# Kernel optimization log

Hardware: AMD Instinct MI355X
Metric: run time of the kernel (lower is better)

Reference implementation:

```python
import jax, jax.numpy as jnp
import numpy as np

SIGMA = 0.1
B = 1.0
EPS = 1e-5


def setup_inputs() -> dict:
    key = jax.random.key(0)
    k1, k2 = jax.random.split(key)
    featureT = jax.random.normal(k1, (2, 256, 64, 64), dtype=jnp.float32)
    featureI = jax.random.normal(k2, (2, 256, 64, 64), dtype=jnp.float32)
    return {"featureT": featureT, "featureI": featureI}


def reference(featureT, featureI):
    # NCHW -> NHWC
    fI = jnp.transpose(featureI, (0, 2, 3, 1))
    fT = jnp.transpose(featureT, (0, 2, 3, 1))
    # center both by target mean over N, H, W (shape [1,1,1,C])
    meanT = fT.mean(axis=(0, 1, 2), keepdims=True)
    fI = fI - meanT
    fT = fT - meanT
    # channelwise L2 normalize
    fI = fI / jnp.linalg.norm(fI, axis=3, keepdims=True)
    fT = fT / jnp.linalg.norm(fT, axis=3, keepdims=True)
    N, H, W, C = fT.shape
    P = H * W
    # conv2d with 1x1 target patches == cosine similarity vs every target patch
    Tp = fT.reshape(N, P, C)                       # [N, P, C]
    dist = jnp.einsum('nhwc,npc->nhwp', fI, Tp)    # [N, H, W, P]
    raw_dist = (1.0 - dist) / 2.0
    # relative distance: divide by min over target-patch axis
    rel = raw_dist / (jnp.min(raw_dist, axis=3, keepdims=True) + EPS)
    # exp weighting, normalized over target-patch axis
    Wt = jnp.exp((B - rel) / SIGMA)
    CX = Wt / Wt.sum(axis=3, keepdims=True)        # [N, H, W, P]
    # max over spatial (query) dims, mean over target patches, -log, mean
    CX = CX.max(axis=2).max(axis=1)                # [N, P]
    CX = -jnp.log(CX.mean(axis=1))                 # [N]
    return jnp.mean(CX)
```

## Files before the change

kernel.cpp:

```cpp
#include <hip/hip_runtime.h>
#include <hip/hip_bf16.h>
#include <math.h>

#define NB 2
#define C 256
#define P 4096
#define EPS_F 1e-5f

typedef __attribute__((ext_vector_type(8))) short short8;
typedef __attribute__((ext_vector_type(4))) float f32x4;

__device__ __forceinline__ float bf2f(unsigned short u) {
    union { unsigned int i; float f; } x;
    x.i = ((unsigned int)u) << 16;
    return x.f;
}

__global__ void k_mean(const float* __restrict__ fT, float* __restrict__ mean) {
    int c = blockIdx.x;
    int t = threadIdx.x;
    const float* p0 = fT + (size_t)c * P;
    const float* p1 = fT + (size_t)(C + c) * P;
    float s = 0.f;
    for (int i = t; i < P; i += 256) s += p0[i] + p1[i];
    __shared__ float red[256];
    red[t] = s; __syncthreads();
    for (int o = 128; o > 0; o >>= 1) { if (t < o) red[t] += red[t + o]; __syncthreads(); }
    if (t == 0) mean[c] = red[0] * (1.f / 8192.f);
}

__global__ __launch_bounds__(256) void k_normpack(const float* __restrict__ fI,
                                                  const float* __restrict__ fT,
                                                  const float* __restrict__ mean,
                                                  __hip_bfloat16* __restrict__ TI,
                                                  __hip_bfloat16* __restrict__ TT) {
    __shared__ float mn[C];
    __shared__ float tile[C][33];
    __shared__ float part[8][32];
    __shared__ float srn[32];
    int t = threadIdx.x;
    const float* f = blockIdx.z ? fT : fI;
    __hip_bfloat16* out = blockIdx.z ? TT : TI;
    mn[t] = mean[t];
    __syncthreads();
    int n = blockIdx.y, p0 = blockIdx.x * 32;
    int pl = t & 31, cg = t >> 5;
    const float* base = f + (size_t)n * C * P + p0 + pl;
    float acc = 0.f;
    #pragma unroll 4
    for (int cc = 0; cc < 32; cc++) {
        int c = cg * 32 + cc;
        float v = base[(size_t)c * P] - mn[c];
        tile[c][pl] = v;
        acc += v * v;
    }
    part[cg][pl] = acc;
    __syncthreads();
    if (t < 32) {
        float s = 0.f;
        #pragma unroll
        for (int g = 0; g < 8; g++) s += part[g][t];
        srn[t] = rsqrtf(s);
    }
    __syncthreads();
    #pragma unroll
    for (int it = 0; it < 4; it++) {
        int flat = it * 2048 + t * 8;
        int p = flat >> 8;
        int c = flat & 255;
        float rn = srn[p];
        union { __hip_bfloat16 h[8]; short8 s; } u;
        #pragma unroll
        for (int k = 0; k < 8; k++)
            u.h[k] = __float2bfloat16(tile[c + k][p] * rn);
        *(short8*)(out + ((size_t)(n * P + p0 + p)) * C + c) = u.s;
    }
}

__device__ __forceinline__ void stage_tile(const __hip_bfloat16* __restrict__ gbase,
                                           __hip_bfloat16* lbuf, int kk, int wid, int lane) {
    #pragma unroll
    for (int j = 0; j < 2; j++) {
        int row = wid * 32 + j * 16 + (lane >> 2);
        int cb = (lane & 3) * 16;
        int scb = cb ^ (((row >> 1) & 3) << 4);
        const char* gp = (const char*)gbase + (size_t)row * (C * 2) + kk * 64 + scb;
        char* lp = (char*)lbuf + (wid * 32 + j * 16) * 64;
        __builtin_amdgcn_global_load_lds(
            (const __attribute__((address_space(1))) void*)gp,
            (__attribute__((address_space(3))) void*)lp, 16, 0, 0);
    }
}

__device__ __forceinline__ short8 ldfrag(const __hip_bfloat16* lbuf, int rloc, int kb) {
    int addr = rloc * 64 + (kb ^ (((rloc >> 1) & 3) << 4));
    return *(const short8*)((const char*)lbuf + addr);
}

__global__ __launch_bounds__(256, 3) void k_gemm(const __hip_bfloat16* __restrict__ TI,
                                                 const __hip_bfloat16* __restrict__ TT,
                                                 __hip_bfloat16* __restrict__ D,
                                                 float* __restrict__ Mpart) {
    __shared__ char smem[49152];
    int lane = threadIdx.x & 63, wid = threadIdx.x >> 6;
    int wr = wid >> 1, wc = wid & 1;
    int n = blockIdx.z;
    const __hip_bfloat16* A = TI + ((size_t)n * P + blockIdx.y * 128) * C;
    const __hip_bfloat16* B = TT + ((size_t)n * P + blockIdx.x * 128) * C;

    f32x4 acc[4][4];
    #pragma unroll
    for (int m = 0; m < 4; m++)
        #pragma unroll
        for (int nt = 0; nt < 4; nt++)
            acc[m][nt] = (f32x4){0.f, 0.f, 0.f, 0.f};

    int rA = lane & 15;
    int kb = (lane >> 4) * 16;

    stage_tile(A, (__hip_bfloat16*)(smem), 0, wid, lane);
    stage_tile(B, (__hip_bfloat16*)(smem + 24576), 0, wid, lane);
    stage_tile(A, (__hip_bfloat16*)(smem + 8192), 1, wid, lane);
    stage_tile(B, (__hip_bfloat16*)(smem + 24576 + 8192), 1, wid, lane);
    asm volatile("s_waitcnt vmcnt(4)" ::: "memory");
    __builtin_amdgcn_s_barrier();
    __builtin_amdgcn_sched_barrier(0);

    #pragma unroll
    for (int t = 0; t < 8; t++) {
        int cur = t % 3;
        if (t < 6) {
            int nxt = (t + 2) % 3;
            stage_tile(A, (__hip_bfloat16*)(smem + nxt * 8192), t + 2, wid, lane);
            stage_tile(B, (__hip_bfloat16*)(smem + 24576 + nxt * 8192), t + 2, wid, lane);
        }
        __hip_bfloat16* lAc = (__hip_bfloat16*)(smem + cur * 8192);
        __hip_bfloat16* lBc = (__hip_bfloat16*)(smem + 24576 + cur * 8192);
        short8 a[4], b[4];
        #pragma unroll
        for (int m = 0; m < 4; m++)
            a[m] = ldfrag(lAc, wr * 64 + m * 16 + rA, kb);
        #pragma unroll
        for (int nt = 0; nt < 4; nt++)
            b[nt] = ldfrag(lBc, wc * 64 + nt * 16 + rA, kb);
        #pragma unroll
        for (int m = 0; m < 4; m++)
            #pragma unroll
            for (int nt = 0; nt < 4; nt++)
                acc[m][nt] = __builtin_amdgcn_mfma_f32_16x16x32_bf16(a[m], b[nt], acc[m][nt], 0, 0, 0);
        if (t < 6)       asm volatile("s_waitcnt vmcnt(4)" ::: "memory");
        else if (t == 6) asm volatile("s_waitcnt vmcnt(0)" ::: "memory");
        __builtin_amdgcn_s_barrier();
        __builtin_amdgcn_sched_barrier(0);
    }

    int rj = (lane >> 4) * 4, cl = lane & 15;
    {
        char* tb = smem;
        #pragma unroll
        for (int m = 0; m < 4; m++)
            #pragma unroll
            for (int nt = 0; nt < 4; nt++)
                #pragma unroll
                for (int j = 0; j < 4; j++) {
                    int row = wr * 64 + m * 16 + rj + j;
                    int colb = (wc * 64 + nt * 16 + cl) * 2;
                    *(__hip_bfloat16*)(tb + row * 256 + (colb ^ (((row >> 2) & 3) << 5))) =
                        __float2bfloat16(acc[m][nt][j]);
                }
        __syncthreads();
        int qb0 = blockIdx.y * 128, pb0 = blockIdx.x * 128;
        char* Dn = (char*)(D + (size_t)n * P * P);
        #pragma unroll
        for (int rb = 0; rb < 8; rb++) {
            int row = wid * 32 + rb * 4 + (lane >> 4);
            int sb = cl * 16;
            short8 v = *(const short8*)(tb + row * 256 + (sb ^ (((row >> 2) & 3) << 5)));
            *(short8*)(Dn + ((size_t)(qb0 + row) * P + pb0) * 2 + sb) = v;
        }
    }

    int qb = blockIdx.y * 128 + wr * 64;
    int pt = blockIdx.x * 2 + wc;
    #pragma unroll
    for (int m = 0; m < 4; m++) {
        f32x4 mx = acc[m][0];
        #pragma unroll
        for (int nt = 1; nt < 4; nt++)
            #pragma unroll
            for (int j = 0; j < 4; j++)
                mx[j] = fmaxf(mx[j], acc[m][nt][j]);
        #pragma unroll
        for (int j = 0; j < 4; j++)
            #pragma unroll
            for (int o = 1; o < 16; o <<= 1)
                mx[j] = fmaxf(mx[j], __shfl_xor(mx[j], o));
        if ((lane & 15) == 0) {
            int qbase = qb + m * 16 + (lane >> 4) * 4;
            #pragma unroll
            for (int j = 0; j < 4; j++)
                Mpart[((size_t)(n * P + qbase + j)) * 64 + pt] = mx[j];
        }
    }
}

__global__ __launch_bounds__(512) void k_zcol(const __hip_bfloat16* __restrict__ D,
                                              const float* __restrict__ Mpart,
                                              float* __restrict__ Cpart) {
    __shared__ float st2[8], sc[8];
    int t = threadIdx.x, lane = t & 63, wv = t >> 6;
    int n = blockIdx.y, g = blockIdx.x;

    float cm[8];
    #pragma unroll
    for (int j = 0; j < 8; j++) cm[j] = -1e30f;

    #pragma unroll
    for (int s = 0; s < 2; s++) {
        int q = g * 16 + s * 8 + wv;
        size_t row = (size_t)n * P + q;
        float m = Mpart[row * 64 + lane];
        #pragma unroll
        for (int o = 32; o > 0; o >>= 1) m = fmaxf(m, __shfl_xor(m, o));
        float t2 = 5.f / ((1.f - m) * 0.5f + EPS_F);

        const short8* src = (const short8*)(D + row * P);
        float z = 0.f;
        #pragma unroll
        for (int k = 0; k < 8; k++) {
            short8 v = src[k * 64 + lane];
            #pragma unroll
            for (int j = 0; j < 8; j++)
                z += __expf(t2 * (bf2f((unsigned short)v[j]) - m));
        }
        #pragma unroll
        for (int o = 32; o > 0; o >>= 1) z += __shfl_xor(z, o);
        if (lane == 0) { st2[wv] = t2; sc[wv] = -t2 * m - logf(z); }
        __syncthreads();

        const __hip_bfloat16* Db = D + ((size_t)n * P + g * 16 + s * 8) * P;
        #pragma unroll
        for (int r = 0; r < 8; r++) {
            short8 v = *(const short8*)(Db + (size_t)r * P + t * 8);
            float tt = st2[r], cc = sc[r];
            #pragma unroll
            for (int j = 0; j < 8; j++)
                cm[j] = fmaxf(cm[j], fmaf(tt, bf2f((unsigned short)v[j]), cc));
        }
        __syncthreads();
    }

    float* cp = Cpart + ((size_t)(n * 256 + g)) * P + t * 8;
    f32x4 v0 = {cm[0], cm[1], cm[2], cm[3]};
    f32x4 v1 = {cm[4], cm[5], cm[6], cm[7]};
    *(f32x4*)cp = v0;
    *(f32x4*)(cp + 4) = v1;
}

__global__ void k_colred1(const float* __restrict__ Cpart, float* __restrict__ Cred2) {
    int np = blockIdx.x * 256 + threadIdx.x;
    int n = np >> 12, p = np & 4095;
    const float* base = Cpart + (size_t)(n * 256) * P + p;
    float c = -1e30f;
    int g0 = blockIdx.y * 32;
    #pragma unroll 8
    for (int g = 0; g < 32; g++)
        c = fmaxf(c, base[(size_t)(g0 + g) * P]);
    Cred2[blockIdx.y * 8192 + np] = c;
}

__global__ void k_colred2(const float* __restrict__ Cred2, float* __restrict__ colmax) {
    int np = blockIdx.x * 256 + threadIdx.x;
    float c = -1e30f;
    #pragma unroll
    for (int y = 0; y < 8; y++)
        c = fmaxf(c, Cred2[y * 8192 + np]);
    colmax[np] = __expf(c);
}

__global__ void k_final(const float* __restrict__ colmax, float* __restrict__ out) {
    __shared__ float red[256];
    int t = threadIdx.x;
    float cx[NB];
    for (int n = 0; n < NB; n++) {
        float s = 0.f;
        for (int i = t; i < P; i += 256) s += colmax[n * P + i];
        red[t] = s; __syncthreads();
        for (int o = 128; o > 0; o >>= 1) { if (t < o) red[t] += red[t + o]; __syncthreads(); }
        cx[n] = -logf(red[0] * (1.f / (float)P));
        __syncthreads();
    }
    if (t == 0) out[0] = 0.5f * (cx[0] + cx[1]);
}

extern "C" void kernel_launch(void* const* d_in, const int* in_sizes, int n_in,
                              void* d_out, int out_size, void* d_ws, size_t ws_size,
                              hipStream_t stream) {
    const float* fT = (const float*)d_in[0];
    const float* fI = (const float*)d_in[1];
    float* out = (float*)d_out;

    char* ws = (char*)d_ws;
    size_t off = 0;
    __hip_bfloat16* TI = (__hip_bfloat16*)(ws + off); off += 4194304;
    __hip_bfloat16* TT = (__hip_bfloat16*)(ws + off); off += 4194304;
    __hip_bfloat16* D  = (__hip_bfloat16*)(ws + off); off += (size_t)NB * P * P * 2;
    float* Mpart  = (float*)(ws + off); off += (size_t)NB * P * 64 * 4;
    float* Cpart  = (float*)(ws + off); off += (size_t)NB * 256 * P * 4;
    float* Cred2  = (float*)(ws + off); off += (size_t)8 * NB * P * 4;
    float* mean   = (float*)(ws + off); off += 1024;
    float* colmax = (float*)(ws + off); off += 32768;

    k_mean<<<256, 256, 0, stream>>>(fT, mean);
    k_normpack<<<dim3(128, 2, 2), 256, 0, stream>>>(fI, fT, mean, TI, TT);
    k_gemm<<<dim3(32, 32, 2), 256, 0, stream>>>(TI, TT, D, Mpart);
    k_zcol<<<dim3(256, 2), 512, 0, stream>>>(D, Mpart, Cpart);
    k_colred1<<<dim3(32, 8), 256, 0, stream>>>(Cpart, Cred2);
    k_colred2<<<32, 256, 0, stream>>>(Cred2, colmax);
    k_final<<<1, 256, 0, stream>>>(colmax, out);
}
```

Baseline: 86.54 us.

## Enlarge GEMM tile to 256 query rows per block to reuse B tiles

```diff
diff --git a/kernel.cpp b/kernel.cpp
--- a/kernel.cpp
+++ b/kernel.cpp
@@ -97,32 +97,37 @@
     return *(const short8*)((const char*)lbuf + addr);
 }
 
-__global__ __launch_bounds__(256, 3) void k_gemm(const __hip_bfloat16* __restrict__ TI,
-                                                 const __hip_bfloat16* __restrict__ TT,
-                                                 __hip_bfloat16* __restrict__ D,
-                                                 float* __restrict__ Mpart) {
-    __shared__ char smem[49152];
+__global__ __launch_bounds__(256) void k_gemm(const __hip_bfloat16* __restrict__ TI,
+                                              const __hip_bfloat16* __restrict__ TT,
+                                              __hip_bfloat16* __restrict__ D,
+                                              float* __restrict__ Mpart) {
+    __shared__ char smem[73728];
     int lane = threadIdx.x & 63, wid = threadIdx.x >> 6;
     int wr = wid >> 1, wc = wid & 1;
     int n = blockIdx.z;
-    const __hip_bfloat16* A = TI + ((size_t)n * P + blockIdx.y * 128) * C;
-    const __hip_bfloat16* B = TT + ((size_t)n * P + blockIdx.x * 128) * C;
-
-    f32x4 acc[4][4];
-    #pragma unroll
-    for (int m = 0; m < 4; m++)
-        #pragma unroll
-        for (int nt = 0; nt < 4; nt++)
-            acc[m][nt] = (f32x4){0.f, 0.f, 0.f, 0.f};
+    const __hip_bfloat16* A0 = TI + ((size_t)n * P + blockIdx.y * 256) * C;
+    const __hip_bfloat16* A1 = A0 + (size_t)128 * C;
+    const __hip_bfloat16* B  = TT + ((size_t)n * P + blockIdx.x * 128) * C;
+
+    f32x4 acc[2][4][4];
+    #pragma unroll
+    for (int qt = 0; qt < 2; qt++)
+        #pragma unroll
+        for (int m = 0; m < 4; m++)
+            #pragma unroll
+            for (int nt = 0; nt < 4; nt++)
+                acc[qt][m][nt] = (f32x4){0.f, 0.f, 0.f, 0.f};
 
     int rA = lane & 15;
     int kb = (lane >> 4) * 16;
 
-    stage_tile(A, (__hip_bfloat16*)(smem), 0, wid, lane);
-    stage_tile(B, (__hip_bfloat16*)(smem + 24576), 0, wid, lane);
-    stage_tile(A, (__hip_bfloat16*)(smem + 8192), 1, wid, lane);
-    stage_tile(B, (__hip_bfloat16*)(smem + 24576 + 8192), 1, wid, lane);
-    asm volatile("s_waitcnt vmcnt(4)" ::: "memory");
+    stage_tile(A0, (__hip_bfloat16*)(smem), 0, wid, lane);
+    stage_tile(A1, (__hip_bfloat16*)(smem + 8192), 0, wid, lane);
+    stage_tile(B,  (__hip_bfloat16*)(smem + 16384), 0, wid, lane);
+    stage_tile(A0, (__hip_bfloat16*)(smem + 24576), 1, wid, lane);
+    stage_tile(A1, (__hip_bfloat16*)(smem + 24576 + 8192), 1, wid, lane);
+    stage_tile(B,  (__hip_bfloat16*)(smem + 24576 + 16384), 1, wid, lane);
+    asm volatile("s_waitcnt vmcnt(6)" ::: "memory");
     __builtin_amdgcn_s_barrier();
     __builtin_amdgcn_sched_barrier(0);
 
@@ -131,32 +136,40 @@
         int cur = t % 3;
         if (t < 6) {
             int nxt = (t + 2) % 3;
-            stage_tile(A, (__hip_bfloat16*)(smem + nxt * 8192), t + 2, wid, lane);
-            stage_tile(B, (__hip_bfloat16*)(smem + 24576 + nxt * 8192), t + 2, wid, lane);
-        }
-        __hip_bfloat16* lAc = (__hip_bfloat16*)(smem + cur * 8192);
-        __hip_bfloat16* lBc = (__hip_bfloat16*)(smem + 24576 + cur * 8192);
-        short8 a[4], b[4];
-        #pragma unroll
-        for (int m = 0; m < 4; m++)
-            a[m] = ldfrag(lAc, wr * 64 + m * 16 + rA, kb);
+            char* nb = smem + nxt * 24576;
+            stage_tile(A0, (__hip_bfloat16*)(nb), t + 2, wid, lane);
+            stage_tile(A1, (__hip_bfloat16*)(nb + 8192), t + 2, wid, lane);
+            stage_tile(B,  (__hip_bfloat16*)(nb + 16384), t + 2, wid, lane);
+        }
+        char* cb = smem + cur * 24576;
+        short8 b[4];
         #pragma unroll
         for (int nt = 0; nt < 4; nt++)
-            b[nt] = ldfrag(lBc, wc * 64 + nt * 16 + rA, kb);
-        #pragma unroll
-        for (int m = 0; m < 4; m++)
-            #pragma unroll
-            for (int nt = 0; nt < 4; nt++)
-                acc[m][nt] = __builtin_amdgcn_mfma_f32_16x16x32_bf16(a[m], b[nt], acc[m][nt], 0, 0, 0);
-        if (t < 6)       asm volatile("s_waitcnt vmcnt(4)" ::: "memory");
+            b[nt] = ldfrag((__hip_bfloat16*)(cb + 16384), wc * 64 + nt * 16 + rA, kb);
+        #pragma unroll
+        for (int qt = 0; qt < 2; qt++) {
+            short8 a[4];
+            #pragma unroll
+            for (int m = 0; m < 4; m++)
+                a[m] = ldfrag((__hip_bfloat16*)(cb + qt * 8192), wr * 64 + m * 16 + rA, kb);
+            #pragma unroll
+            for (int m = 0; m < 4; m++)
+                #pragma unroll
+                for (int nt = 0; nt < 4; nt++)
+                    acc[qt][m][nt] = __builtin_amdgcn_mfma_f32_16x16x32_bf16(a[m], b[nt], acc[qt][m][nt], 0, 0, 0);
+        }
+        if (t < 6)       asm volatile("s_waitcnt vmcnt(6)" ::: "memory");
         else if (t == 6) asm volatile("s_waitcnt vmcnt(0)" ::: "memory");
         __builtin_amdgcn_s_barrier();
         __builtin_amdgcn_sched_barrier(0);
     }
 
     int rj = (lane >> 4) * 4, cl = lane & 15;
-    {
-        char* tb = smem;
+    char* tb = smem;
+    int pb0 = blockIdx.x * 128;
+    char* Dn = (char*)(D + (size_t)n * P * P);
+    #pragma unroll
+    for (int qt = 0; qt < 2; qt++) {
         #pragma unroll
         for (int m = 0; m < 4; m++)
             #pragma unroll
@@ -166,11 +179,10 @@
                     int row = wr * 64 + m * 16 + rj + j;
                     int colb = (wc * 64 + nt * 16 + cl) * 2;
                     *(__hip_bfloat16*)(tb + row * 256 + (colb ^ (((row >> 2) & 3) << 5))) =
-                        __float2bfloat16(acc[m][nt][j]);
+                        __float2bfloat16(acc[qt][m][nt][j]);
                 }
         __syncthreads();
-        int qb0 = blockIdx.y * 128, pb0 = blockIdx.x * 128;
-        char* Dn = (char*)(D + (size_t)n * P * P);
+        int qb0 = blockIdx.y * 256 + qt * 128;
         #pragma unroll
         for (int rb = 0; rb < 8; rb++) {
             int row = wid * 32 + rb * 4 + (lane >> 4);
@@ -178,28 +190,32 @@
             short8 v = *(const short8*)(tb + row * 256 + (sb ^ (((row >> 2) & 3) << 5)));
             *(short8*)(Dn + ((size_t)(qb0 + row) * P + pb0) * 2 + sb) = v;
         }
-    }
-
-    int qb = blockIdx.y * 128 + wr * 64;
+        __syncthreads();
+    }
+
     int pt = blockIdx.x * 2 + wc;
     #pragma unroll
-    for (int m = 0; m < 4; m++) {
-        f32x4 mx = acc[m][0];
-        #pragma unroll
-        for (int nt = 1; nt < 4; nt++)
+    for (int qt = 0; qt < 2; qt++) {
+        int qb = blockIdx.y * 256 + qt * 128 + wr * 64;
+        #pragma unroll
+        for (int m = 0; m < 4; m++) {
+            f32x4 mx = acc[qt][m][0];
+            #pragma unroll
+            for (int nt = 1; nt < 4; nt++)
+                #pragma unroll
+                for (int j = 0; j < 4; j++)
+                    mx[j] = fmaxf(mx[j], acc[qt][m][nt][j]);
             #pragma unroll
             for (int j = 0; j < 4; j++)
-                mx[j] = fmaxf(mx[j], acc[m][nt][j]);
-        #pragma unroll
-        for (int j = 0; j < 4; j++)
-            #pragma unroll
-            for (int o = 1; o < 16; o <<= 1)
-                mx[j] = fmaxf(mx[j], __shfl_xor(mx[j], o));
-        if ((lane & 15) == 0) {
-            int qbase = qb + m * 16 + (lane >> 4) * 4;
-            #pragma unroll
-            for (int j = 0; j < 4; j++)
-                Mpart[((size_t)(n * P + qbase + j)) * 64 + pt] = mx[j];
+                #pragma unroll
+                for (int o = 1; o < 16; o <<= 1)
+                    mx[j] = fmaxf(mx[j], __shfl_xor(mx[j], o));
+            if ((lane & 15) == 0) {
+                int qbase = qb + m * 16 + (lane >> 4) * 4;
+                #pragma unroll
+                for (int j = 0; j < 4; j++)
+                    Mpart[((size_t)(n * P + qbase + j)) * 64 + pt] = mx[j];
+            }
         }
     }
 }
@@ -313,7 +329,7 @@
 
     k_mean<<<256, 256, 0, stream>>>(fT, mean);
     k_normpack<<<dim3(128, 2, 2), 256, 0, stream>>>(fI, fT, mean, TI, TT);
-    k_gemm<<<dim3(32, 32, 2), 256, 0, stream>>>(TI, TT, D, Mpart);
+    k_gemm<<<dim3(32, 16, 2), 256, 0, stream>>>(TI, TT, D, Mpart);
     k_zcol<<<dim3(256, 2), 512, 0, stream>>>(D, Mpart, Cpart);
     k_colred1<<<dim3(32, 8), 256, 0, stream>>>(Cpart, Cred2);
     k_colred2<<<32, 256, 0, stream>>>(Cred2, colmax);
```

New measurement: 99.22 us. +14.7%, slower.
